# Performance work log

Measured on AMD Instinct MI355X. Metric: run time of the kernel, lower is better.

Reference implementation:

```python
import jax, jax.numpy as jnp
import numpy as np

B, T, D = 256, 400, 280
H, L, K = 384, 12, 10
CHUNK = H // L
G = 4 * H + 2 * L  # gate projection width


def setup_inputs() -> dict:
    key = jax.random.key(0)
    ks = jax.random.split(key, 16)
    s = 0.02
    return {
        "x": jax.random.normal(ks[0], (B, T, D), jnp.float32),
        "time": jax.random.uniform(ks[1], (B, T), jnp.float32),
        "Wk": jax.random.normal(ks[2], (D + 1, G), jnp.float32) * s,
        "bk": jnp.zeros((G,), jnp.float32),
        "Wr": jax.random.normal(ks[3], (H + 1, G), jnp.float32) * s,
        "br": jnp.zeros((G,), jnp.float32),
        "Ws": jax.random.normal(ks[4], (H, H // 6), jnp.float32) * s,
        "bs": jnp.zeros((H // 6,), jnp.float32),
        "Wrs": jax.random.normal(ks[5], (H // 6, H), jnp.float32) * s,
        "brs": jnp.zeros((H,), jnp.float32),
        "Wc": jax.random.normal(ks[6], (H, H, K), jnp.float32) * s,  # Conv1d (out,in,kernel)
        "bc": jnp.zeros((H,), jnp.float32),
        "Wo": jax.random.normal(ks[7], (H, 1), jnp.float32) * s,
        "bo": jnp.zeros((1,), jnp.float32),
    }


def _cumax_l2r(z):
    return jnp.cumsum(jax.nn.softmax(z, axis=-1), axis=-1)


def _cumax_r2l(z):
    zf = jnp.flip(z, axis=-1)
    return jnp.flip(jnp.cumsum(jax.nn.softmax(zf, axis=-1), axis=-1), axis=-1)


def _stagenet(x, time, Wk, bk, Wr, br, Ws, bs, Wrs, brs, Wc, bc, Wo, bo):
    b = x.shape[0]

    def step(carry, xt):
        c, h = carry
        x_t, tm = xt  # (B,D), (B,)
        tm1 = tm[:, None]
        xo = (jnp.concatenate([x_t, tm1], axis=-1) @ Wk + bk
              + jnp.concatenate([h, tm1], axis=-1) @ Wr + br)  # (B, G)
        fm = _cumax_l2r(xo[:, :L])[:, :, None]          # (B,L,1) f master gate
        im = _cumax_r2l(xo[:, L:2 * L])[:, :, None]     # (B,L,1) i master gate
        g = xo[:, 2 * L:].reshape(b, 4 * L, CHUNK)
        f = jax.nn.sigmoid(g[:, :L])
        i = jax.nn.sigmoid(g[:, L:2 * L])
        o = jax.nn.sigmoid(g[:, 2 * L:3 * L])
        c_in = jnp.tanh(g[:, 3 * L:])
        cl = c.reshape(b, L, CHUNK)
        ov = fm * im
        c_new = ov * (f * cl + i * c_in) + (fm - ov) * cl + (im - ov) * c_in
        h_new = (o * jnp.tanh(c_new)).reshape(b, H)
        c_new = c_new.reshape(b, H)
        dist = 1.0 - jnp.mean(fm[..., 0], axis=-1)  # (B,)
        return (c_new, h_new), (h_new, dist)

    init = (jnp.zeros((b, H), x.dtype), jnp.zeros((b, H), x.dtype))
    (c_fin, h_fin), (h_all, dis_all) = jax.lax.scan(
        step, init, (x.swapaxes(0, 1), time.T))

    tmp_h = h_all[-K:]      # (K,B,H) last conv_size hidden states
    tmp_dis = dis_all[-K:]  # (K,B)
    local_dis = jax.nn.softmax(jnp.cumsum(tmp_dis.T, axis=1), axis=1)  # (B,K)
    local_h = tmp_h.transpose(1, 2, 0) * local_dis[:, None, :]          # (B,H,K)

    theme = jax.nn.sigmoid(
        jax.nn.relu(jnp.mean(local_h, axis=-1) @ Ws + bs) @ Wrs + brs)  # (B,H)
    conv = jnp.einsum('bck,ock->bo', local_h, Wc) + bc                   # (B,H)
    lh = theme * conv
    rnn_output = lh + h_fin
    out = jax.nn.sigmoid(rnn_output @ Wo + bo).reshape(b)
    return out


def reference(x, time, Wk, bk, Wr, br, Ws, bs, Wrs, brs, Wc, bc, Wo, bo):
    return _stagenet(x, time, Wk, bk, Wr, br, Ws, bs, Wrs, brs, Wc, bc, Wo, bo)
```

## Files before the change

kernel.cpp:

```cpp
#include <hip/hip_runtime.h>
#include <hip/hip_bf16.h>
#include <stdint.h>

#define B_  256
#define T_  400
#define D_  280
#define H_  384
#define L_  12
#define K_  10
#define G_  1560
#define NP_ 1568
#define NT_USED 98
#define NT_PAD  104

typedef __attribute__((ext_vector_type(8))) short  short8_t;
typedef __attribute__((ext_vector_type(4))) float  float4_t;

__device__ __forceinline__ unsigned short f2bf(float f) {
  union { __hip_bfloat16 h; unsigned short u; } cv;
  cv.h = __float2bfloat16(f);
  return cv.u;
}
__device__ __forceinline__ float bf2f_lo(uint32_t u) { return __uint_as_float(u << 16); }
__device__ __forceinline__ float bf2f_hi(uint32_t u) { return __uint_as_float(u & 0xffff0000u); }
__device__ __forceinline__ float sigm(float x) { return 1.f / (1.f + __expf(-x)); }

__device__ __forceinline__ int perm_g(int p) {
  if (p < 0 || p >= 32 + 12 * 128) return -1;
  if (p < 24) return p;
  if (p < 32) return -1;
  int q = p - 32;
  int l = q >> 7, r = q & 127, jb = r >> 5, cc = r & 31;
  return 24 + ((jb * 12 + l) << 5) + cc;
}

__global__ void k_build_wkbf(const float* __restrict__ Wk, const float* __restrict__ bk,
                             const float* __restrict__ Wr, const float* __restrict__ br,
                             uint4* __restrict__ wkbF, float* __restrict__ bias) {
  int idx  = blockIdx.x * 256 + threadIdx.x;
  int lane = idx & 63;
  int rest = idx >> 6;
  int kt = rest % 9, nt = rest / 9;
  if (nt >= NT_PAD) return;
  int p = nt * 16 + (lane & 15);
  int g = perm_g(p);
  int kbase = kt * 32 + ((lane >> 4) << 3);
  unsigned short v[8];
#pragma unroll
  for (int j = 0; j < 8; ++j) {
    int k = kbase + j;
    float val = 0.f;
    if (g >= 0) {
      if (k < 280)        val = Wk[(size_t)k * G_ + g];
      else if (k == 280)  val = Wk[(size_t)280 * G_ + g] + Wr[(size_t)384 * G_ + g];
    }
    v[j] = f2bf(val);
  }
  uint4 u;
  u.x = (uint32_t)v[0] | ((uint32_t)v[1] << 16);
  u.y = (uint32_t)v[2] | ((uint32_t)v[3] << 16);
  u.z = (uint32_t)v[4] | ((uint32_t)v[5] << 16);
  u.w = (uint32_t)v[6] | ((uint32_t)v[7] << 16);
  wkbF[(size_t)(nt * 9 + kt) * 64 + lane] = u;
  if (kt == 0 && (lane >> 4) == 0 && p < NP_)
    bias[p] = (g >= 0) ? (bk[g] + br[g]) : 0.f;
}

__global__ void k_build_wrf(const float* __restrict__ Wr, uint4* __restrict__ wrF) {
  int idx  = blockIdx.x * 256 + threadIdx.x;
  int lane = idx & 63;
  int rest = idx >> 6;
  int kt = rest % 12, nt = rest / 12;
  if (nt >= NT_USED) return;
  int p = nt * 16 + (lane & 15);
  int g = perm_g(p);
  int kbase = kt * 32 + ((lane >> 4) << 3);
  unsigned short v[8];
#pragma unroll
  for (int j = 0; j < 8; ++j) {
    int k = kbase + j;
    float val = (g >= 0) ? Wr[(size_t)k * G_ + g] : 0.f;
    v[j] = f2bf(val);
  }
  uint4 u;
  u.x = (uint32_t)v[0] | ((uint32_t)v[1] << 16);
  u.y = (uint32_t)v[2] | ((uint32_t)v[3] << 16);
  u.z = (uint32_t)v[4] | ((uint32_t)v[5] << 16);
  u.w = (uint32_t)v[6] | ((uint32_t)v[7] << 16);
  wrF[(size_t)(nt * 12 + kt) * 64 + lane] = u;
}

__global__ __launch_bounds__(256) void k_pre_gemm(
    const float* __restrict__ x, const float* __restrict__ timev,
    const uint4* __restrict__ wkbF, const float* __restrict__ bias,
    uint2* __restrict__ preF) {
  __shared__ unsigned short A_lds[128 * 40];
  __shared__ uint4 B_lds[8 * 64];
  const int tid = threadIdx.x;
  const int ntile = blockIdx.x;
  const int tm = blockIdx.y;
  const int t = tm >> 1, b0 = (tm & 1) << 7;
  const int wv = tid >> 6, lane = tid & 63;
  const int wr = wv >> 1, wc = wv & 1;
  float4_t acc[4][4];
#pragma unroll
  for (int fi = 0; fi < 4; ++fi)
#pragma unroll
    for (int fj = 0; fj < 4; ++fj) { acc[fi][fj][0]=0.f; acc[fi][fj][1]=0.f; acc[fi][fj][2]=0.f; acc[fi][fj][3]=0.f; }

  for (int kt = 0; kt < 9; ++kt) {
    {
      int mi = tid >> 1, half = tid & 1, kk0 = half * 16;
      int b = b0 + mi;
      const float* xrow = x + ((size_t)b * T_ + t) * D_;
      int k0 = kt * 32 + kk0;
      unsigned short* dst = &A_lds[mi * 40 + kk0];
      if (kt < 8) {
        float4 v0 = *(const float4*)(xrow + k0);
        float4 v1 = *(const float4*)(xrow + k0 + 4);
        float4 v2 = *(const float4*)(xrow + k0 + 8);
        float4 v3 = *(const float4*)(xrow + k0 + 12);
        dst[0]=f2bf(v0.x); dst[1]=f2bf(v0.y); dst[2]=f2bf(v0.z); dst[3]=f2bf(v0.w);
        dst[4]=f2bf(v1.x); dst[5]=f2bf(v1.y); dst[6]=f2bf(v1.z); dst[7]=f2bf(v1.w);
        dst[8]=f2bf(v2.x); dst[9]=f2bf(v2.y); dst[10]=f2bf(v2.z); dst[11]=f2bf(v2.w);
        dst[12]=f2bf(v3.x); dst[13]=f2bf(v3.y); dst[14]=f2bf(v3.z); dst[15]=f2bf(v3.w);
      } else {
#pragma unroll
        for (int e = 0; e < 16; ++e) {
          int k = k0 + e;
          float val = 0.f;
          if (k < 280)       val = xrow[k];
          else if (k == 280) val = timev[(size_t)b * T_ + t];
          dst[e] = f2bf(val);
        }
      }
    }
#pragma unroll
    for (int pz = 0; pz < 2; ++pz) {
      int fn = (tid >> 6) + pz * 4;
      int inner = tid & 63;
      int ntg = ntile * 8 + fn;
      B_lds[fn * 64 + inner] = wkbF[(size_t)(ntg * 9 + kt) * 64 + inner];
    }
    __syncthreads();
    short8_t a[4], bfr[4];
#pragma unroll
    for (int fi = 0; fi < 4; ++fi) {
      int m = wr * 64 + fi * 16 + (lane & 15);
      a[fi] = *(const short8_t*)&A_lds[m * 40 + ((lane >> 4) << 3)];
    }
#pragma unroll
    for (int fj = 0; fj < 4; ++fj) {
      uint4 u = B_lds[(wc * 4 + fj) * 64 + lane];
      bfr[fj] = *reinterpret_cast<short8_t*>(&u);
    }
#pragma unroll
    for (int fi = 0; fi < 4; ++fi)
#pragma unroll
      for (int fj = 0; fj < 4; ++fj)
        acc[fi][fj] = __builtin_amdgcn_mfma_f32_16x16x32_bf16(a[fi], bfr[fj], acc[fi][fj], 0, 0, 0);
    __syncthreads();
  }
#pragma unroll
  for (int fi = 0; fi < 4; ++fi)
#pragma unroll
    for (int fj = 0; fj < 4; ++fj) {
      int nt_g = ntile * 8 + wc * 4 + fj;
      if (nt_g < NT_USED) {
        int bg = (b0 >> 4) + wr * 4 + fi;
        float bv = bias[nt_g * 16 + (lane & 15)];
        unsigned short r0 = f2bf(acc[fi][fj][0] + bv);
        unsigned short r1 = f2bf(acc[fi][fj][1] + bv);
        unsigned short r2 = f2bf(acc[fi][fj][2] + bv);
        unsigned short r3 = f2bf(acc[fi][fj][3] + bv);
        uint2 u;
        u.x = (uint32_t)r0 | ((uint32_t)r1 << 16);
        u.y = (uint32_t)r2 | ((uint32_t)r3 << 16);
        preF[(((size_t)t * 16 + bg) * NT_USED + nt_g) * 64 + lane] = u;
      }
    }
}

#define XOS 164
__global__ __launch_bounds__(256)
__attribute__((amdgpu_waves_per_eu(1, 1)))
void k_scan(
    const uint2* __restrict__ preF, const uint4* __restrict__ wrF,
    uint32_t* __restrict__ hbuf, uint32_t* __restrict__ flags,
    float* __restrict__ hist_h, float* __restrict__ hist_dis) {
  __shared__ float xoL[16][XOS];
  __shared__ float cSt[16][32];
  __shared__ float fmv[16], imv[16];
  const int tid  = threadIdx.x;
  const int wv   = tid >> 6, lane = tid & 63;
  const int bid  = blockIdx.x;
  const int l_own = bid >> 4, bg = bid & 15;
  int ltg[3], ntg[3];
  ltg[0] = wv; ltg[1] = 4 + wv; ltg[2] = 8 + wv;
#pragma unroll
  for (int i = 0; i < 3; ++i) {
    int lt = ltg[i];
    int nn = (lt < 2) ? lt : (2 + 8 * l_own + (lt - 2));
    ntg[i] = (nn < NT_USED && lt < 10) ? nn : 0;
  }
  short8_t wrf[3][12];
#pragma unroll
  for (int i = 0; i < 3; ++i) {
#pragma unroll
    for (int kt = 0; kt < 12; ++kt) {
      uint4 u = wrF[(size_t)(ntg[i] * 12 + kt) * 64 + lane];
      wrf[i][kt] = *reinterpret_cast<short8_t*>(&u);
    }
  }
  { int b = tid >> 4, cp = tid & 15; cSt[b][cp * 2] = 0.f; cSt[b][cp * 2 + 1] = 0.f; }
  __syncthreads();

  const int rr0 = lane >> 4;
  const int cN  = lane & 15;
  for (int t = 0; t < T_; ++t) {
    float4_t acc[3];
#pragma unroll
    for (int i = 0; i < 3; ++i) {
      uint2 p = preF[(((size_t)t * 16 + bg) * NT_USED + ntg[i]) * 64 + lane];
      acc[i][0] = bf2f_lo(p.x); acc[i][1] = bf2f_hi(p.x);
      acc[i][2] = bf2f_lo(p.y); acc[i][3] = bf2f_hi(p.y);
    }
    if (t > 0) {
      const uint32_t need = (uint32_t)t;
      int budget = 50000;
      bool ok = false;
      while (!ok && budget-- > 0) {
        uint32_t mn = 0xffffffffu;
#pragma unroll
        for (int q = 0; q < 12; ++q) {
          uint32_t v = __hip_atomic_load(flags + (bg * 12 + q) * 16,
                                         __ATOMIC_RELAXED, __HIP_MEMORY_SCOPE_AGENT);
          mn = (v < mn) ? v : mn;
        }
        ok = (mn >= need);
      }
    }
    __builtin_amdgcn_sched_barrier(0);
    asm volatile("" ::: "memory");
    const int slot = t & 1;
    short8_t af[12];
#pragma unroll
    for (int kt = 0; kt < 12; ++kt) {
      const unsigned long long* hp =
          (const unsigned long long*)(hbuf + (((slot * 16 + bg) * 12 + kt) << 8) + lane * 4);
      unsigned long long u0 = __hip_atomic_load(hp + 0, __ATOMIC_RELAXED, __HIP_MEMORY_SCOPE_AGENT);
      unsigned long long u1 = __hip_atomic_load(hp + 1, __ATOMIC_RELAXED, __HIP_MEMORY_SCOPE_AGENT);
      uint4 u;
      u.x = (uint32_t)u0; u.y = (uint32_t)(u0 >> 32);
      u.z = (uint32_t)u1; u.w = (uint32_t)(u1 >> 32);
      af[kt] = *reinterpret_cast<short8_t*>(&u);
    }
#pragma unroll
    for (int kt = 0; kt < 12; ++kt) {
#pragma unroll
      for (int i = 0; i < 3; ++i)
        acc[i] = __builtin_amdgcn_mfma_f32_16x16x32_bf16(af[kt], wrf[i][kt], acc[i], 0, 0, 0);
    }
#pragma unroll
    for (int i = 0; i < 3; ++i) {
      if (ltg[i] < 10) {
#pragma unroll
        for (int r = 0; r < 4; ++r)
          xoL[rr0 * 4 + r][ltg[i] * 16 + cN] = acc[i][r];
      }
    }
    __syncthreads();
    if (tid < 32) {
      int b = tid & 15;
      int base = (tid < 16) ? 0 : 12;
      float v[12], mx = -1e30f;
#pragma unroll
      for (int j = 0; j < 12; ++j) { v[j] = xoL[b][base + j]; mx = fmaxf(mx, v[j]); }
      float e[12], s = 0.f;
#pragma unroll
      for (int j = 0; j < 12; ++j) { e[j] = __expf(v[j] - mx); s += e[j]; }
      float inv = 1.f / s;
      if (tid < 16) {
        float cum = 0.f, fml = 0.f, fsum = 0.f;
#pragma unroll
        for (int j = 0; j < 12; ++j) {
          cum += e[j] * inv;
          if (j == l_own) fml = cum;
          fsum += cum;
        }
        fmv[b] = fml;
        if (l_own == 0 && t >= T_ - K_)
          hist_dis[(t - (T_ - K_)) * B_ + bg * 16 + b] = 1.f - fsum * (1.f / 12.f);
      } else {
        float cum = 0.f, iml = 0.f;
#pragma unroll
        for (int j = 11; j >= 0; --j) {
          cum += e[j] * inv;
          if (j == l_own) iml = cum;
        }
        imv[b] = iml;
      }
    }
    __syncthreads();
    {
      int b = tid >> 4, cp = tid & 15, c0 = cp << 1;
      float fm_ = fmv[b], im_ = imv[b], ov = fm_ * im_;
      uint32_t packed = 0;
      float hh[2];
#pragma unroll
      for (int e2 = 0; e2 < 2; ++e2) {
        int c = c0 + e2;
        float f  = sigm(xoL[b][32 + c]);
        float ii = sigm(xoL[b][64 + c]);
        float oo = sigm(xoL[b][96 + c]);
        float ci = tanhf(xoL[b][128 + c]);
        float cl = cSt[b][c];
        float cn = ov * (f * cl + ii * ci) + (fm_ - ov) * cl + (im_ - ov) * ci;
        cSt[b][c] = cn;
        float h = oo * tanhf(cn);
        hh[e2] = h;
        packed |= (uint32_t)f2bf(h) << (16 * e2);
      }
      int hl = b + ((c0 >> 3) << 4);
      int slot2 = (t + 1) & 1;
      uint32_t* hp = hbuf + (((slot2 * 16 + bg) * 12 + l_own) << 8) + hl * 4 + ((c0 & 7) >> 1);
      __hip_atomic_store(hp, packed, __ATOMIC_RELAXED, __HIP_MEMORY_SCOPE_AGENT);
      if (t >= T_ - K_) {
        float* hd = hist_h + (((size_t)(t - (T_ - K_)) * B_) + bg * 16 + b) * H_ + l_own * 32 + c0;
        hd[0] = hh[0]; hd[1] = hh[1];
      }
    }
    __syncthreads();
    if (tid == 0 && t < T_ - 1)
      __hip_atomic_store(flags + (bg * 12 + l_own) * 16, (uint32_t)(t + 1),
                         __ATOMIC_RELAXED, __HIP_MEMORY_SCOPE_AGENT);
  }
}

__global__ void k_epi1(const float* __restrict__ hist_dis, const float* __restrict__ hist_h,
                       const float* __restrict__ Ws, const float* __restrict__ bs,
                       const float* __restrict__ Wrs, const float* __restrict__ brs,
                       float* __restrict__ ldis, float* __restrict__ theme) {
  int b = blockIdx.x, tid = threadIdx.x;
  __shared__ float ld_s[K_], mh[H_], t1[64];
  if (tid == 0) {
    float cum = 0.f, v[K_], mx = -1e30f;
#pragma unroll
    for (int k = 0; k < K_; ++k) { cum += hist_dis[k * B_ + b]; v[k] = cum; mx = fmaxf(mx, cum); }
    float e[K_], s = 0.f;
#pragma unroll
    for (int k = 0; k < K_; ++k) { e[k] = __expf(v[k] - mx); s += e[k]; }
    float inv = 1.f / s;
#pragma unroll
    for (int k = 0; k < K_; ++k) { float r = e[k] * inv; ld_s[k] = r; ldis[b * K_ + k] = r; }
  }
  __syncthreads();
  for (int h = tid; h < H_; h += 64) {
    float a = 0.f;
#pragma unroll
    for (int k = 0; k < K_; ++k) a += hist_h[((size_t)k * B_ + b) * H_ + h] * ld_s[k];
    mh[h] = a * 0.1f;
  }
  __syncthreads();
  {
    float a = bs[tid];
    for (int h = 0; h < H_; ++h) a += mh[h] * Ws[h * 64 + tid];
    t1[tid] = fmaxf(a, 0.f);
  }
  __syncthreads();
  for (int o = tid; o < H_; o += 64) {
    float a = brs[o];
#pragma unroll 8
    for (int j = 0; j < 64; ++j) a += t1[j] * Wrs[j * H_ + o];
    theme[b * H_ + o] = sigm(a);
  }
}

__global__ __launch_bounds__(256) void k_epi2(const float* __restrict__ hist_h,
                                              const float* __restrict__ ldis,
                                              const float* __restrict__ Wc,
                                              const float* __restrict__ bc,
                                              float* __restrict__ convb) {
  __shared__ float lh_s[16][644];
  int og = blockIdx.x, bgp = blockIdx.y, tid = threadIdx.x;
  int b_l = tid & 15, o_l = tid >> 4;
  int b = bgp * 16 + b_l, o = og * 16 + o_l;
  float acc = 0.f;
  for (int c0 = 0; c0 < H_; c0 += 64) {
    __syncthreads();
    for (int it = tid; it < 16 * 64 * K_; it += 256) {
      int bb = it / 640, rem = it % 640, cc = rem / K_, k = rem % K_;
      lh_s[bb][cc * K_ + k] =
          hist_h[((size_t)k * B_ + bgp * 16 + bb) * H_ + c0 + cc] * ldis[(bgp * 16 + bb) * K_ + k];
    }
    __syncthreads();
    const float* wp = Wc + ((size_t)o * H_ + c0) * K_;
    for (int cc = 0; cc < 64; ++cc) {
#pragma unroll
      for (int k = 0; k < K_; ++k) acc += lh_s[b_l][cc * K_ + k] * wp[cc * K_ + k];
    }
  }
  convb[b * H_ + o] = acc + bc[o];
}

__global__ void k_epi3(const float* __restrict__ theme, const float* __restrict__ convb,
                       const float* __restrict__ hist_h, const float* __restrict__ Wo,
                       const float* __restrict__ bo, float* __restrict__ out) {
  int b = blockIdx.x, tid = threadIdx.x;
  __shared__ float part[6];
  float hfin = hist_h[((size_t)(K_ - 1) * B_ + b) * H_ + tid];
  float v = (theme[b * H_ + tid] * convb[b * H_ + tid] + hfin) * Wo[tid];
#pragma unroll
  for (int off = 32; off >= 1; off >>= 1) v += __shfl_down(v, off, 64);
  if ((tid & 63) == 0) part[tid >> 6] = v;
  __syncthreads();
  if (tid == 0) {
    float s = part[0] + part[1] + part[2] + part[3] + part[4] + part[5];
    out[b] = sigm(s + bo[0]);
  }
}

extern "C" void kernel_launch(void* const* d_in, const int* in_sizes, int n_in,
                              void* d_out, int out_size, void* d_ws, size_t ws_size,
                              hipStream_t stream) {
  const float* x    = (const float*)d_in[0];
  const float* tmv  = (const float*)d_in[1];
  const float* Wk   = (const float*)d_in[2];
  const float* bk   = (const float*)d_in[3];
  const float* Wr   = (const float*)d_in[4];
  const float* br   = (const float*)d_in[5];
  const float* Ws   = (const float*)d_in[6];
  const float* bs   = (const float*)d_in[7];
  const float* Wrs  = (const float*)d_in[8];
  const float* brs  = (const float*)d_in[9];
  const float* Wc   = (const float*)d_in[10];
  const float* bc   = (const float*)d_in[11];
  const float* Wo   = (const float*)d_in[12];
  const float* bo   = (const float*)d_in[13];

  char* ws = (char*)d_ws;
  size_t off = 0;
  auto alloc = [&](size_t bytes) { size_t o = off; off = (off + bytes + 255) & ~(size_t)255; return o; };
  const size_t PREF_B  = (size_t)T_ * 16 * NT_USED * 512;
  const size_t WKBF_B  = (size_t)NT_PAD * 9 * 1024;
  const size_t WRF_B   = (size_t)NT_USED * 12 * 1024;
  const size_t BIAS_B  = (size_t)NP_ * 4;
  const size_t HBUF_B  = (size_t)2 * 16 * 12 * 1024;
  const size_t FLAG_B  = (size_t)192 * 64;
  const size_t HISTH_B = (size_t)K_ * B_ * H_ * 4;
  const size_t HISTD_B = (size_t)K_ * B_ * 4;
  const size_t LDIS_B  = (size_t)B_ * K_ * 4;
  const size_t THEME_B = (size_t)B_ * H_ * 4;
  const size_t CONV_B  = (size_t)B_ * H_ * 4;

  size_t o_pref  = alloc(PREF_B);
  size_t o_wkbf  = alloc(WKBF_B);
  size_t o_wrf   = alloc(WRF_B);
  size_t o_bias  = alloc(BIAS_B);
  size_t o_hbuf  = alloc(HBUF_B + FLAG_B);
  size_t o_flag  = o_hbuf + HBUF_B;
  size_t o_hh    = alloc(HISTH_B);
  size_t o_hd    = alloc(HISTD_B);
  size_t o_ld    = alloc(LDIS_B);
  size_t o_th    = alloc(THEME_B);
  size_t o_cv    = alloc(CONV_B);
  if (ws_size < off) return;

  uint2*    preF  = (uint2*)(ws + o_pref);
  uint4*    wkbF  = (uint4*)(ws + o_wkbf);
  uint4*    wrF   = (uint4*)(ws + o_wrf);
  float*    bias  = (float*)(ws + o_bias);
  uint32_t* hbuf  = (uint32_t*)(ws + o_hbuf);
  uint32_t* flags = (uint32_t*)(ws + o_flag);
  float*    histh = (float*)(ws + o_hh);
  float*    histd = (float*)(ws + o_hd);
  float*    ldis  = (float*)(ws + o_ld);
  float*    theme = (float*)(ws + o_th);
  float*    convb = (float*)(ws + o_cv);

  hipMemsetAsync(ws + o_hbuf, 0, HBUF_B + FLAG_B, stream);
  k_build_wkbf<<<(NT_PAD * 9 * 64) / 256, 256, 0, stream>>>(Wk, bk, Wr, br, wkbF, bias);
  k_build_wrf<<<(NT_USED * 12 * 64) / 256, 256, 0, stream>>>(Wr, wrF);
  k_pre_gemm<<<dim3(13, T_ * 2), 256, 0, stream>>>(x, tmv, wkbF, bias, preF);
  k_scan<<<192, 256, 0, stream>>>(preF, wrF, hbuf, flags, histh, histd);
  k_epi1<<<B_, 64, 0, stream>>>(histd, histh, Ws, bs, Wrs, brs, ldis, theme);
  k_epi2<<<dim3(24, 16), 256, 0, stream>>>(histh, ldis, Wc, bc, convb);
  k_epi3<<<B_, 384, 0, stream>>>(theme, convb, histh, Wo, bo, (float*)d_out);
}
```

Baseline: 2.275 ms.

## Process two batch groups per scan block, halving grid and cross-block sync

The recurrent scan kernel now has each block handle two batch groups, so the grid shrinks from 192 to 96 blocks. Each block reuses its register-resident recurrent weight fragments for twice the MFMA work and waits on both groups' flags. tanhf is also replaced with an exp-based fast tanh, and the waves_per_eu attribute becomes launch_bounds(256,1). This aims to amortize per-step sync and latency over more work, at the cost of more registers, per-block serial work, and slight accuracy loss from the fast tanh.

Measured after the change: 2.859 ms. +25.7%, slower.

```diff
diff --git a/kernel.cpp b/kernel.cpp
--- a/kernel.cpp
+++ b/kernel.cpp
@@ -24,6 +24,7 @@
 __device__ __forceinline__ float bf2f_lo(uint32_t u) { return __uint_as_float(u << 16); }
 __device__ __forceinline__ float bf2f_hi(uint32_t u) { return __uint_as_float(u & 0xffff0000u); }
 __device__ __forceinline__ float sigm(float x) { return 1.f / (1.f + __expf(-x)); }
+__device__ __forceinline__ float ftanh(float x) { return 1.f - 2.f / (__expf(2.f * x) + 1.f); }
 
 __device__ __forceinline__ int perm_g(int p) {
   if (p < 0 || p >= 32 + 12 * 128) return -1;
@@ -182,19 +183,18 @@
 }
 
 #define XOS 164
-__global__ __launch_bounds__(256)
-__attribute__((amdgpu_waves_per_eu(1, 1)))
+__global__ __launch_bounds__(256, 1)
 void k_scan(
     const uint2* __restrict__ preF, const uint4* __restrict__ wrF,
     uint32_t* __restrict__ hbuf, uint32_t* __restrict__ flags,
     float* __restrict__ hist_h, float* __restrict__ hist_dis) {
-  __shared__ float xoL[16][XOS];
-  __shared__ float cSt[16][32];
-  __shared__ float fmv[16], imv[16];
+  __shared__ float xoL[2][16][XOS];
+  __shared__ float cSt[2][16][32];
+  __shared__ float fmv[2][16], imv[2][16];
   const int tid  = threadIdx.x;
   const int wv   = tid >> 6, lane = tid & 63;
   const int bid  = blockIdx.x;
-  const int l_own = bid >> 4, bg = bid & 15;
+  const int l_own = bid >> 3, bgp = bid & 7;
   int ltg[3], ntg[3];
   ltg[0] = wv; ltg[1] = 4 + wv; ltg[2] = 8 + wv;
 #pragma unroll
@@ -212,18 +212,24 @@
       wrf[i][kt] = *reinterpret_cast<short8_t*>(&u);
     }
   }
-  { int b = tid >> 4, cp = tid & 15; cSt[b][cp * 2] = 0.f; cSt[b][cp * 2 + 1] = 0.f; }
+  { int b = tid >> 4, cp = tid & 15;
+    cSt[0][b][cp * 2] = 0.f; cSt[0][b][cp * 2 + 1] = 0.f;
+    cSt[1][b][cp * 2] = 0.f; cSt[1][b][cp * 2 + 1] = 0.f; }
   __syncthreads();
 
   const int rr0 = lane >> 4;
   const int cN  = lane & 15;
   for (int t = 0; t < T_; ++t) {
-    float4_t acc[3];
-#pragma unroll
-    for (int i = 0; i < 3; ++i) {
-      uint2 p = preF[(((size_t)t * 16 + bg) * NT_USED + ntg[i]) * 64 + lane];
-      acc[i][0] = bf2f_lo(p.x); acc[i][1] = bf2f_hi(p.x);
-      acc[i][2] = bf2f_lo(p.y); acc[i][3] = bf2f_hi(p.y);
+    float4_t acc[2][3];
+#pragma unroll
+    for (int cx = 0; cx < 2; ++cx) {
+      int bg = bgp + 8 * cx;
+#pragma unroll
+      for (int i = 0; i < 3; ++i) {
+        uint2 p = preF[(((size_t)t * 16 + bg) * NT_USED + ntg[i]) * 64 + lane];
+        acc[cx][i][0] = bf2f_lo(p.x); acc[cx][i][1] = bf2f_hi(p.x);
+        acc[cx][i][2] = bf2f_lo(p.y); acc[cx][i][3] = bf2f_hi(p.y);
+      }
     }
     if (t > 0) {
       const uint32_t need = (uint32_t)t;
@@ -233,8 +239,11 @@
         uint32_t mn = 0xffffffffu;
 #pragma unroll
         for (int q = 0; q < 12; ++q) {
-          uint32_t v = __hip_atomic_load(flags + (bg * 12 + q) * 16,
-                                         __ATOMIC_RELAXED, __HIP_MEMORY_SCOPE_AGENT);
+          uint32_t vA = __hip_atomic_load(flags + (bgp * 12 + q) * 16,
+                                          __ATOMIC_RELAXED, __HIP_MEMORY_SCOPE_AGENT);
+          uint32_t vB = __hip_atomic_load(flags + ((bgp + 8) * 12 + q) * 16,
+                                          __ATOMIC_RELAXED, __HIP_MEMORY_SCOPE_AGENT);
+          uint32_t v = (vA < vB) ? vA : vB;
           mn = (v < mn) ? v : mn;
         }
         ok = (mn >= need);
@@ -243,44 +252,54 @@
     __builtin_amdgcn_sched_barrier(0);
     asm volatile("" ::: "memory");
     const int slot = t & 1;
-    short8_t af[12];
+    short8_t af[2][12];
+#pragma unroll
+    for (int cx = 0; cx < 2; ++cx) {
+      int bg = bgp + 8 * cx;
+#pragma unroll
+      for (int kt = 0; kt < 12; ++kt) {
+        const unsigned long long* hp =
+            (const unsigned long long*)(hbuf + (((slot * 16 + bg) * 12 + kt) << 8) + lane * 4);
+        unsigned long long u0 = __hip_atomic_load(hp + 0, __ATOMIC_RELAXED, __HIP_MEMORY_SCOPE_AGENT);
+        unsigned long long u1 = __hip_atomic_load(hp + 1, __ATOMIC_RELAXED, __HIP_MEMORY_SCOPE_AGENT);
+        uint4 u;
+        u.x = (uint32_t)u0; u.y = (uint32_t)(u0 >> 32);
+        u.z = (uint32_t)u1; u.w = (uint32_t)(u1 >> 32);
+        af[cx][kt] = *reinterpret_cast<short8_t*>(&u);
+      }
+    }
 #pragma unroll
     for (int kt = 0; kt < 12; ++kt) {
-      const unsigned long long* hp =
-          (const unsigned long long*)(hbuf + (((slot * 16 + bg) * 12 + kt) << 8) + lane * 4);
-      unsigned long long u0 = __hip_atomic_load(hp + 0, __ATOMIC_RELAXED, __HIP_MEMORY_SCOPE_AGENT);
-      unsigned long long u1 = __hip_atomic_load(hp + 1, __ATOMIC_RELAXED, __HIP_MEMORY_SCOPE_AGENT);
-      uint4 u;
-      u.x = (uint32_t)u0; u.y = (uint32_t)(u0 >> 32);
-      u.z = (uint32_t)u1; u.w = (uint32_t)(u1 >> 32);
-      af[kt] = *reinterpret_cast<short8_t*>(&u);
-    }
-#pragma unroll
-    for (int kt = 0; kt < 12; ++kt) {
-#pragma unroll
-      for (int i = 0; i < 3; ++i)
-        acc[i] = __builtin_amdgcn_mfma_f32_16x16x32_bf16(af[kt], wrf[i][kt], acc[i], 0, 0, 0);
-    }
-#pragma unroll
-    for (int i = 0; i < 3; ++i) {
-      if (ltg[i] < 10) {
-#pragma unroll
-        for (int r = 0; r < 4; ++r)
-          xoL[rr0 * 4 + r][ltg[i] * 16 + cN] = acc[i][r];
-      }
-    }
-    __syncthreads();
-    if (tid < 32) {
-      int b = tid & 15;
-      int base = (tid < 16) ? 0 : 12;
+#pragma unroll
+      for (int cx = 0; cx < 2; ++cx)
+#pragma unroll
+        for (int i = 0; i < 3; ++i)
+          acc[cx][i] = __builtin_amdgcn_mfma_f32_16x16x32_bf16(af[cx][kt], wrf[i][kt], acc[cx][i], 0, 0, 0);
+    }
+#pragma unroll
+    for (int cx = 0; cx < 2; ++cx)
+#pragma unroll
+      for (int i = 0; i < 3; ++i) {
+        if (ltg[i] < 10) {
+#pragma unroll
+          for (int r = 0; r < 4; ++r)
+            xoL[cx][rr0 * 4 + r][ltg[i] * 16 + cN] = acc[cx][i][r];
+        }
+      }
+    __syncthreads();
+    if (tid < 64) {
+      int cx  = tid >> 5;
+      int sub = tid & 31;
+      int b = sub & 15;
+      int base = (sub < 16) ? 0 : 12;
       float v[12], mx = -1e30f;
 #pragma unroll
-      for (int j = 0; j < 12; ++j) { v[j] = xoL[b][base + j]; mx = fmaxf(mx, v[j]); }
+      for (int j = 0; j < 12; ++j) { v[j] = xoL[cx][b][base + j]; mx = fmaxf(mx, v[j]); }
       float e[12], s = 0.f;
 #pragma unroll
       for (int j = 0; j < 12; ++j) { e[j] = __expf(v[j] - mx); s += e[j]; }
       float inv = 1.f / s;
-      if (tid < 16) {
+      if (sub < 16) {
         float cum = 0.f, fml = 0.f, fsum = 0.f;
 #pragma unroll
         for (int j = 0; j < 12; ++j) {
@@ -288,9 +307,9 @@
           if (j == l_own) fml = cum;
           fsum += cum;
         }
-        fmv[b] = fml;
+        fmv[cx][b] = fml;
         if (l_own == 0 && t >= T_ - K_)
-          hist_dis[(t - (T_ - K_)) * B_ + bg * 16 + b] = 1.f - fsum * (1.f / 12.f);
+          hist_dis[(t - (T_ - K_)) * B_ + (bgp + 8 * cx) * 16 + b] = 1.f - fsum * (1.f / 12.f);
       } else {
         float cum = 0.f, iml = 0.f;
 #pragma unroll
@@ -298,42 +317,54 @@
           cum += e[j] * inv;
           if (j == l_own) iml = cum;
         }
-        imv[b] = iml;
-      }
-    }
-    __syncthreads();
+        imv[cx][b] = iml;
+      }
+    }
+    __syncthreads();
+    float hist0[2], hist1[2];
     {
       int b = tid >> 4, cp = tid & 15, c0 = cp << 1;
-      float fm_ = fmv[b], im_ = imv[b], ov = fm_ * im_;
-      uint32_t packed = 0;
-      float hh[2];
-#pragma unroll
-      for (int e2 = 0; e2 < 2; ++e2) {
-        int c = c0 + e2;
-        float f  = sigm(xoL[b][32 + c]);
-        float ii = sigm(xoL[b][64 + c]);
-        float oo = sigm(xoL[b][96 + c]);
-        float ci = tanhf(xoL[b][128 + c]);
-        float cl = cSt[b][c];
-        float cn = ov * (f * cl + ii * ci) + (fm_ - ov) * cl + (im_ - ov) * ci;
-        cSt[b][c] = cn;
-        float h = oo * tanhf(cn);
-        hh[e2] = h;
-        packed |= (uint32_t)f2bf(h) << (16 * e2);
-      }
-      int hl = b + ((c0 >> 3) << 4);
       int slot2 = (t + 1) & 1;
-      uint32_t* hp = hbuf + (((slot2 * 16 + bg) * 12 + l_own) << 8) + hl * 4 + ((c0 & 7) >> 1);
-      __hip_atomic_store(hp, packed, __ATOMIC_RELAXED, __HIP_MEMORY_SCOPE_AGENT);
-      if (t >= T_ - K_) {
-        float* hd = hist_h + (((size_t)(t - (T_ - K_)) * B_) + bg * 16 + b) * H_ + l_own * 32 + c0;
-        hd[0] = hh[0]; hd[1] = hh[1];
-      }
-    }
-    __syncthreads();
-    if (tid == 0 && t < T_ - 1)
-      __hip_atomic_store(flags + (bg * 12 + l_own) * 16, (uint32_t)(t + 1),
+#pragma unroll
+      for (int cx = 0; cx < 2; ++cx) {
+        float fm_ = fmv[cx][b], im_ = imv[cx][b], ov = fm_ * im_;
+        uint32_t packed = 0;
+        float hh[2];
+#pragma unroll
+        for (int e2 = 0; e2 < 2; ++e2) {
+          int c = c0 + e2;
+          float f  = sigm(xoL[cx][b][32 + c]);
+          float ii = sigm(xoL[cx][b][64 + c]);
+          float oo = sigm(xoL[cx][b][96 + c]);
+          float ci = ftanh(xoL[cx][b][128 + c]);
+          float cl = cSt[cx][b][c];
+          float cn = ov * (f * cl + ii * ci) + (fm_ - ov) * cl + (im_ - ov) * ci;
+          cSt[cx][b][c] = cn;
+          float h = oo * ftanh(cn);
+          hh[e2] = h;
+          packed |= (uint32_t)f2bf(h) << (16 * e2);
+        }
+        hist0[cx] = hh[0]; hist1[cx] = hh[1];
+        int hl = b + ((c0 >> 3) << 4);
+        uint32_t* hp = hbuf + (((slot2 * 16 + (bgp + 8 * cx)) * 12 + l_own) << 8) + hl * 4 + ((c0 & 7) >> 1);
+        __hip_atomic_store(hp, packed, __ATOMIC_RELAXED, __HIP_MEMORY_SCOPE_AGENT);
+      }
+    }
+    __syncthreads();
+    if (tid == 0 && t < T_ - 1) {
+      __hip_atomic_store(flags + (bgp * 12 + l_own) * 16, (uint32_t)(t + 1),
                          __ATOMIC_RELAXED, __HIP_MEMORY_SCOPE_AGENT);
+      __hip_atomic_store(flags + ((bgp + 8) * 12 + l_own) * 16, (uint32_t)(t + 1),
+                         __ATOMIC_RELAXED, __HIP_MEMORY_SCOPE_AGENT);
+    }
+    if (t >= T_ - K_) {
+      int b = tid >> 4, cp = tid & 15, c0 = cp << 1;
+#pragma unroll
+      for (int cx = 0; cx < 2; ++cx) {
+        float* hd = hist_h + (((size_t)(t - (T_ - K_)) * B_) + (bgp + 8 * cx) * 16 + b) * H_ + l_own * 32 + c0;
+        hd[0] = hist0[cx]; hd[1] = hist1[cx];
+      }
+    }
   }
 }
 
@@ -482,7 +513,7 @@
   k_build_wkbf<<<(NT_PAD * 9 * 64) / 256, 256, 0, stream>>>(Wk, bk, Wr, br, wkbF, bias);
   k_build_wrf<<<(NT_USED * 12 * 64) / 256, 256, 0, stream>>>(Wr, wrF);
   k_pre_gemm<<<dim3(13, T_ * 2), 256, 0, stream>>>(x, tmv, wkbF, bias, preF);
-  k_scan<<<192, 256, 0, stream>>>(preF, wrF, hbuf, flags, histh, histd);
+  k_scan<<<96, 256, 0, stream>>>(preF, wrF, hbuf, flags, histh, histd);
   k_epi1<<<B_, 64, 0, stream>>>(histd, histh, Ws, bs, Wrs, brs, ldis, theme);
   k_epi2<<<dim3(24, 16), 256, 0, stream>>>(histh, ldis, Wc, bc, convb);
   k_epi3<<<B_, 384, 0, stream>>>(theme, convb, histh, Wo, bo, (float*)d_out);
```

## Use per-wave progress flags with lane-parallel polling in recurrent scan

Applied to the files above, without the earlier changes.

Each wave now publishes its own progress flag right after its hidden-state stores drain, instead of one flag per block after a block barrier. Consumers poll all 48 flags of a batch group at once, one flag per lane, combined with a wave vote, replacing a serial 12-load loop. This shortens the critical path of the cross-block handoff on every timestep. It also swaps tanhf for an exp-based fast tanh, keeps the weight fragments pinned in registers, and packs the flags densely, which raises contention on shared cache lines and slightly changes numerics.

Result: slower. 2.559 ms (+12.5%).

```diff
diff --git a/kernel.cpp b/kernel.cpp
--- a/kernel.cpp
+++ b/kernel.cpp
@@ -24,6 +24,7 @@
 __device__ __forceinline__ float bf2f_lo(uint32_t u) { return __uint_as_float(u << 16); }
 __device__ __forceinline__ float bf2f_hi(uint32_t u) { return __uint_as_float(u & 0xffff0000u); }
 __device__ __forceinline__ float sigm(float x) { return 1.f / (1.f + __expf(-x)); }
+__device__ __forceinline__ float ftanh(float x) { return 1.f - 2.f / (__expf(2.f * x) + 1.f); }
 
 __device__ __forceinline__ int perm_g(int p) {
   if (p < 0 || p >= 32 + 12 * 128) return -1;
@@ -182,8 +183,7 @@
 }
 
 #define XOS 164
-__global__ __launch_bounds__(256)
-__attribute__((amdgpu_waves_per_eu(1, 1)))
+__global__ __launch_bounds__(256, 1)
 void k_scan(
     const uint2* __restrict__ preF, const uint4* __restrict__ wrF,
     uint32_t* __restrict__ hbuf, uint32_t* __restrict__ flags,
@@ -209,6 +209,7 @@
 #pragma unroll
     for (int kt = 0; kt < 12; ++kt) {
       uint4 u = wrF[(size_t)(ntg[i] * 12 + kt) * 64 + lane];
+      asm volatile("" : "+v"(u.x), "+v"(u.y), "+v"(u.z), "+v"(u.w));
       wrf[i][kt] = *reinterpret_cast<short8_t*>(&u);
     }
   }
@@ -217,6 +218,7 @@
 
   const int rr0 = lane >> 4;
   const int cN  = lane & 15;
+  const int qpoll = (lane < 48) ? lane : (lane - 48);
   for (int t = 0; t < T_; ++t) {
     float4_t acc[3];
 #pragma unroll
@@ -227,17 +229,12 @@
     }
     if (t > 0) {
       const uint32_t need = (uint32_t)t;
-      int budget = 50000;
+      const uint32_t* fp = flags + bg * 48 + qpoll;
+      int budget = 200000;
       bool ok = false;
       while (!ok && budget-- > 0) {
-        uint32_t mn = 0xffffffffu;
-#pragma unroll
-        for (int q = 0; q < 12; ++q) {
-          uint32_t v = __hip_atomic_load(flags + (bg * 12 + q) * 16,
-                                         __ATOMIC_RELAXED, __HIP_MEMORY_SCOPE_AGENT);
-          mn = (v < mn) ? v : mn;
-        }
-        ok = (mn >= need);
+        uint32_t v = __hip_atomic_load(fp, __ATOMIC_RELAXED, __HIP_MEMORY_SCOPE_AGENT);
+        ok = __all(v >= need);
       }
     }
     __builtin_amdgcn_sched_barrier(0);
@@ -302,6 +299,7 @@
       }
     }
     __syncthreads();
+    float hh0, hh1;
     {
       int b = tid >> 4, cp = tid & 15, c0 = cp << 1;
       float fm_ = fmv[b], im_ = imv[b], ov = fm_ * im_;
@@ -313,27 +311,30 @@
         float f  = sigm(xoL[b][32 + c]);
         float ii = sigm(xoL[b][64 + c]);
         float oo = sigm(xoL[b][96 + c]);
-        float ci = tanhf(xoL[b][128 + c]);
+        float ci = ftanh(xoL[b][128 + c]);
         float cl = cSt[b][c];
         float cn = ov * (f * cl + ii * ci) + (fm_ - ov) * cl + (im_ - ov) * ci;
         cSt[b][c] = cn;
-        float h = oo * tanhf(cn);
+        float h = oo * ftanh(cn);
         hh[e2] = h;
         packed |= (uint32_t)f2bf(h) << (16 * e2);
       }
+      hh0 = hh[0]; hh1 = hh[1];
       int hl = b + ((c0 >> 3) << 4);
       int slot2 = (t + 1) & 1;
       uint32_t* hp = hbuf + (((slot2 * 16 + bg) * 12 + l_own) << 8) + hl * 4 + ((c0 & 7) >> 1);
       __hip_atomic_store(hp, packed, __ATOMIC_RELAXED, __HIP_MEMORY_SCOPE_AGENT);
-      if (t >= T_ - K_) {
-        float* hd = hist_h + (((size_t)(t - (T_ - K_)) * B_) + bg * 16 + b) * H_ + l_own * 32 + c0;
-        hd[0] = hh[0]; hd[1] = hh[1];
-      }
-    }
-    __syncthreads();
-    if (tid == 0 && t < T_ - 1)
-      __hip_atomic_store(flags + (bg * 12 + l_own) * 16, (uint32_t)(t + 1),
+    }
+    asm volatile("s_waitcnt vmcnt(0)" ::: "memory");
+    if ((tid & 63) == 0 && t < T_ - 1)
+      __hip_atomic_store(flags + bg * 48 + l_own * 4 + wv, (uint32_t)(t + 1),
                          __ATOMIC_RELAXED, __HIP_MEMORY_SCOPE_AGENT);
+    if (t >= T_ - K_) {
+      int b = tid >> 4, cp = tid & 15, c0 = cp << 1;
+      float* hd = hist_h + (((size_t)(t - (T_ - K_)) * B_) + bg * 16 + b) * H_ + l_own * 32 + c0;
+      hd[0] = hh0; hd[1] = hh1;
+    }
+    __syncthreads();
   }
 }
 
@@ -446,7 +447,7 @@
   const size_t WRF_B   = (size_t)NT_USED * 12 * 1024;
   const size_t BIAS_B  = (size_t)NP_ * 4;
   const size_t HBUF_B  = (size_t)2 * 16 * 12 * 1024;
-  const size_t FLAG_B  = (size_t)192 * 64;
+  const size_t FLAG_B  = (size_t)4096;
   const size_t HISTH_B = (size_t)K_ * B_ * H_ * 4;
   const size_t HISTD_B = (size_t)K_ * B_ * 4;
   const size_t LDIS_B  = (size_t)B_ * K_ * 4;
```
